# Kernel tuning notes

Hardware: AMD Instinct MI355X
Metric: run time of the kernel (lower is better)

Reference implementation:

```python
import jax, jax.numpy as jnp
import numpy as np

GROUP_SIZE = 64
SCALING = 1.0  # lora_alpha / r = 16 / 16
# bitsandbytes NF4 codebook (16 normal-float levels)
NF4_CODE = jnp.array([
    -1.0, -0.6961928009986877, -0.5250730514526367, -0.39491748809814453,
    -0.28444138169288635, -0.18477343022823334, -0.09105003625154495, 0.0,
    0.07958029955625534, 0.16093020141124725, 0.24611230194568634,
    0.33791524171829224, 0.44070982933044434, 0.5626170039176941,
    0.7229568362236023, 1.0], dtype=jnp.float32)

IN_F, OUT_F, R, TOKENS = 4096, 11008, 16, 32


def setup_inputs() -> dict:
    key = jax.random.key(0)
    k0, k1, k2, k3, k4 = jax.random.split(key, 5)
    x = jax.random.normal(k0, (TOKENS, IN_F), dtype=jnp.float32)
    # each byte packs two 4-bit NF4 indices (high nibble first)
    packed_weight = jax.random.randint(k1, (OUT_F * IN_F // 2,), 0, 256, dtype=jnp.int32)
    # per-group absmax scales (positive)
    scales = jax.random.uniform(k2, (OUT_F * IN_F // GROUP_SIZE,), dtype=jnp.float32,
                                minval=0.005, maxval=0.05)
    lora_A = jax.random.normal(k3, (R, IN_F), dtype=jnp.float32) * 0.02
    lora_B = jax.random.normal(k4, (OUT_F, R), dtype=jnp.float32) * 0.02
    return {"x": x, "packed_weight": packed_weight, "scales": scales,
            "lora_A": lora_A, "lora_B": lora_B}


def _dequant_nf4(packed_weight, scales):
    hi = packed_weight // 16          # first nibble
    lo = packed_weight % 16           # second nibble
    idx = jnp.stack([hi, lo], axis=-1).reshape(-1)          # [out*in]
    w = NF4_CODE[idx].reshape(-1, GROUP_SIZE) * scales[:, None]
    return w.reshape(OUT_F, IN_F)                            # [out, in]


def reference(x, packed_weight, scales, lora_A, lora_B):
    W = _dequant_nf4(packed_weight, scales)
    base = x @ W.T                                           # [tokens, out]
    lora = (x @ lora_A.T) @ lora_B.T                         # low-rank update
    return base + SCALING * lora
```

## Files before the change

### kernel.cpp

```cpp
#include <hip/hip_runtime.h>
#include <hip/hip_bf16.h>

#define IN_F 4096
#define OUT_F 11008
#define TOKENS 32
#define RANK 16
#define KSPLIT 8
#define KSLICE (IN_F / KSPLIT)
#define XPAD 520
#define OUT_ELEMS (TOKENS * OUT_F)

typedef unsigned short u16;
typedef __attribute__((ext_vector_type(8))) short bf16x8;
typedef __attribute__((ext_vector_type(4))) float f32x4;
typedef __attribute__((ext_vector_type(4))) int i32x4;

__device__ const float NF4_d[16] = {
    -1.0f, -0.6961928009986877f, -0.5250730514526367f, -0.39491748809814453f,
    -0.28444138169288635f, -0.18477343022823334f, -0.09105003625154495f, 0.0f,
    0.07958029955625534f, 0.16093020141124725f, 0.24611230194568634f,
    0.33791524171829224f, 0.44070982933044434f, 0.5626170039176941f,
    0.7229568362236023f, 1.0f};

static __device__ __forceinline__ unsigned pk2(float a, float b) {
    __hip_bfloat162 h = __float22bfloat162_rn(make_float2(a, b));
    unsigned u;
    __builtin_memcpy(&u, &h, 4);
    return u;
}

__global__ void prep_xa_zero(const float* __restrict__ x, const float* __restrict__ A,
                             float* __restrict__ xa, float* __restrict__ out) {
    __shared__ float red[256];
    if (blockIdx.x >= 512) {
        int i = (blockIdx.x - 512) * 256 + threadIdx.x;
        float4 z = make_float4(0.f, 0.f, 0.f, 0.f);
        for (int j = i; j < OUT_ELEMS / 4; j += 16384) ((float4*)out)[j] = z;
        return;
    }
    int b = blockIdx.x;
    int t = b >> 4, r = b & 15;
    const float4* xr = (const float4*)(x + t * IN_F);
    const float4* ar = (const float4*)(A + r * IN_F);
    float s = 0.f;
    for (int c = 0; c < 4; ++c) {
        int j = c * 256 + threadIdx.x;
        float4 xv = xr[j], av = ar[j];
        s += xv.x * av.x + xv.y * av.y + xv.z * av.z + xv.w * av.w;
    }
    red[threadIdx.x] = s;
    __syncthreads();
    for (int st = 128; st > 0; st >>= 1) {
        if (threadIdx.x < st) red[threadIdx.x] += red[threadIdx.x + st];
        __syncthreads();
    }
    if (threadIdx.x == 0) xa[b] = red[0];
}

__global__ __launch_bounds__(256, 4) void qlora_fused(
    const int* __restrict__ packed, const float* __restrict__ scales,
    const float* __restrict__ x, const float* __restrict__ xa,
    const float* __restrict__ B, float* __restrict__ out) {
    __shared__ u16 xs[32 * XPAD];
    __shared__ unsigned tbl[256];
    __shared__ float xal[512];
    const int tid = threadIdx.x;
    const int kbase = blockIdx.y * KSLICE;
    const int obase = blockIdx.x * 64;

    const int lane = tid & 63;
    const int wv = tid >> 6;
    const int n = lane & 15;
    const int q = lane >> 4;
    const int o = obase + wv * 16 + n;

    const i32x4* ppq = (const i32x4*)(packed + o * 2048 + (kbase >> 1)) + q;
    i32x4 P[4];
    P[0] = __builtin_nontemporal_load(ppq);
    P[1] = __builtin_nontemporal_load(ppq + 4);
    P[2] = __builtin_nontemporal_load(ppq + 8);
    P[3] = __builtin_nontemporal_load(ppq + 12);

    const float4* sp = (const float4*)(scales + o * 64 + (kbase >> 6));
    float4 sA = sp[0], sB = sp[1];

    tbl[tid] = pk2(NF4_d[tid & 15], NF4_d[tid >> 4]);

    if (blockIdx.y == 0) {
        xal[tid] = xa[tid];
        xal[tid + 256] = xa[tid + 256];
    }

    for (int it = 0; it < 8; ++it) {
        int row = it * 4 + (tid >> 6);
        int c8 = tid & 63;
        const float4* src = (const float4*)(x + row * IN_F + kbase + c8 * 8);
        float4 v0 = src[0], v1 = src[1];
        uint4 d;
        d.x = pk2(v0.x, v0.y);
        d.y = pk2(v0.z, v0.w);
        d.z = pk2(v1.x, v1.y);
        d.w = pk2(v1.z, v1.w);
        *(uint4*)(xs + row * XPAD + c8 * 8) = d;
    }
    __syncthreads();

    f32x4 acc0 = {0.f, 0.f, 0.f, 0.f};
    f32x4 acc1 = {0.f, 0.f, 0.f, 0.f};
    const u16* xr0 = xs + n * XPAD + q * 8;
    const u16* xr1 = xs + (n + 16) * XPAD + q * 8;
    const float scr[8] = {sA.x, sA.y, sA.z, sA.w, sB.x, sB.y, sB.z, sB.w};

#pragma unroll
    for (int s = 0; s < 16; ++s) {
        i32x4 cur = P[s & 3];
        if (s + 4 < 16) P[s & 3] = __builtin_nontemporal_load(ppq + (s + 4) * 4);
        float sc = scr[s >> 1];

        unsigned u0 = tbl[cur[0] & 255];
        unsigned u1 = tbl[cur[1] & 255];
        unsigned u2 = tbl[cur[2] & 255];
        unsigned u3 = tbl[cur[3] & 255];
        uint4 bu;
        bu.x = pk2(__int_as_float(u0 & 0xFFFF0000u) * sc, __int_as_float(u0 << 16) * sc);
        bu.y = pk2(__int_as_float(u1 & 0xFFFF0000u) * sc, __int_as_float(u1 << 16) * sc);
        bu.z = pk2(__int_as_float(u2 & 0xFFFF0000u) * sc, __int_as_float(u2 << 16) * sc);
        bu.w = pk2(__int_as_float(u3 & 0xFFFF0000u) * sc, __int_as_float(u3 << 16) * sc);
        bf16x8 bfrag;
        __builtin_memcpy(&bfrag, &bu, 16);
        bf16x8 a0 = *(const bf16x8*)(xr0 + s * 32);
        bf16x8 a1 = *(const bf16x8*)(xr1 + s * 32);
        acc0 = __builtin_amdgcn_mfma_f32_16x16x32_bf16(a0, bfrag, acc0, 0, 0, 0);
        acc1 = __builtin_amdgcn_mfma_f32_16x16x32_bf16(a1, bfrag, acc1, 0, 0, 0);
    }

    float lora[8] = {0.f, 0.f, 0.f, 0.f, 0.f, 0.f, 0.f, 0.f};
    if (blockIdx.y == 0) {
        const float4* br = (const float4*)(B + o * RANK);
        float4 b0 = br[0], b1 = br[1], b2 = br[2], b3 = br[3];
#pragma unroll
        for (int r = 0; r < 4; ++r) {
            const float* x0 = xal + (q * 4 + r) * RANK;
            const float* x1 = xal + (q * 4 + r + 16) * RANK;
            float s0 = 0.f, s1 = 0.f;
#pragma unroll
            for (int j = 0; j < 4; ++j) {
                const float4 bj = ((const float4*)&b0)[0];
            }
            s0 = b0.x * x0[0] + b0.y * x0[1] + b0.z * x0[2] + b0.w * x0[3] +
                 b1.x * x0[4] + b1.y * x0[5] + b1.z * x0[6] + b1.w * x0[7] +
                 b2.x * x0[8] + b2.y * x0[9] + b2.z * x0[10] + b2.w * x0[11] +
                 b3.x * x0[12] + b3.y * x0[13] + b3.z * x0[14] + b3.w * x0[15];
            s1 = b0.x * x1[0] + b0.y * x1[1] + b0.z * x1[2] + b0.w * x1[3] +
                 b1.x * x1[4] + b1.y * x1[5] + b1.z * x1[6] + b1.w * x1[7] +
                 b2.x * x1[8] + b2.y * x1[9] + b2.z * x1[10] + b2.w * x1[11] +
                 b3.x * x1[12] + b3.y * x1[13] + b3.z * x1[14] + b3.w * x1[15];
            lora[r] = s0;
            lora[r + 4] = s1;
        }
    }

#pragma unroll
    for (int r = 0; r < 4; ++r) {
        int t = q * 4 + r;
        atomicAdd(out + t * OUT_F + o, acc0[r] + lora[r]);
        atomicAdd(out + (t + 16) * OUT_F + o, acc1[r] + lora[r + 4]);
    }
}

extern "C" void kernel_launch(void* const* d_in, const int* in_sizes, int n_in,
                              void* d_out, int out_size, void* d_ws, size_t ws_size,
                              hipStream_t stream) {
    const float* x = (const float*)d_in[0];
    const int* packed = (const int*)d_in[1];
    const float* scales = (const float*)d_in[2];
    const float* lora_A = (const float*)d_in[3];
    const float* lora_B = (const float*)d_in[4];
    float* out = (float*)d_out;

    float* xa = (float*)d_ws;

    prep_xa_zero<<<576, 256, 0, stream>>>(x, lora_A, xa, out);
    qlora_fused<<<dim3(OUT_F / 64, KSPLIT), 256, 0, stream>>>(packed, scales, x, xa,
                                                              lora_B, out);
}
```

Baseline: 152.2 us.

## Pre-convert x to bf16, load via LDS DMA, replace atomics with split-K reduction

```diff
diff --git a/kernel.cpp b/kernel.cpp
--- a/kernel.cpp
+++ b/kernel.cpp
@@ -9,6 +9,7 @@
 #define KSLICE (IN_F / KSPLIT)
 #define XPAD 520
 #define OUT_ELEMS (TOKENS * OUT_F)
+#define NBLK (OUT_F / 64)
 
 typedef unsigned short u16;
 typedef __attribute__((ext_vector_type(8))) short bf16x8;
@@ -29,15 +30,29 @@
     return u;
 }
 
-__global__ void prep_xa_zero(const float* __restrict__ x, const float* __restrict__ A,
-                             float* __restrict__ xa, float* __restrict__ out) {
-    __shared__ float red[256];
-    if (blockIdx.x >= 512) {
-        int i = (blockIdx.x - 512) * 256 + threadIdx.x;
+__global__ void prep_kernel(const float* __restrict__ x, const float* __restrict__ A,
+                            float* __restrict__ xa, u16* __restrict__ xb,
+                            float* __restrict__ out) {
+    if (blockIdx.x >= 528) {
+        int i = (blockIdx.x - 528) * 256 + threadIdx.x;
         float4 z = make_float4(0.f, 0.f, 0.f, 0.f);
         for (int j = i; j < OUT_ELEMS / 4; j += 16384) ((float4*)out)[j] = z;
         return;
     }
+    if (blockIdx.x >= 512) {
+        int i = (blockIdx.x - 512) * 256 + threadIdx.x;
+#pragma unroll
+        for (int j = 0; j < 8; ++j) {
+            int idx = j * 4096 + i;
+            float4 v = ((const float4*)x)[idx];
+            uint2 d;
+            d.x = pk2(v.x, v.y);
+            d.y = pk2(v.z, v.w);
+            ((uint2*)xb)[idx] = d;
+        }
+        return;
+    }
+    __shared__ float red[256];
     int b = blockIdx.x;
     int t = b >> 4, r = b & 15;
     const float4* xr = (const float4*)(x + t * IN_F);
@@ -57,10 +72,11 @@
     if (threadIdx.x == 0) xa[b] = red[0];
 }
 
+template <int MODE>
 __global__ __launch_bounds__(256, 4) void qlora_fused(
     const int* __restrict__ packed, const float* __restrict__ scales,
-    const float* __restrict__ x, const float* __restrict__ xa,
-    const float* __restrict__ B, float* __restrict__ out) {
+    const u16* __restrict__ xb, const float* __restrict__ xa,
+    const float* __restrict__ B, float* __restrict__ outp) {
     __shared__ u16 xs[32 * XPAD];
     __shared__ unsigned tbl[256];
     __shared__ float xal[512];
@@ -84,24 +100,23 @@
     const float4* sp = (const float4*)(scales + o * 64 + (kbase >> 6));
     float4 sA = sp[0], sB = sp[1];
 
-    tbl[tid] = pk2(NF4_d[tid & 15], NF4_d[tid >> 4]);
-
-    if (blockIdx.y == 0) {
+    tbl[tid] = pk2(NF4_d[tid >> 4], NF4_d[tid & 15]);
+
+    if (MODE == 1 && blockIdx.y == 0) {
         xal[tid] = xa[tid];
         xal[tid + 256] = xa[tid + 256];
     }
 
-    for (int it = 0; it < 8; ++it) {
-        int row = it * 4 + (tid >> 6);
-        int c8 = tid & 63;
-        const float4* src = (const float4*)(x + row * IN_F + kbase + c8 * 8);
-        float4 v0 = src[0], v1 = src[1];
-        uint4 d;
-        d.x = pk2(v0.x, v0.y);
-        d.y = pk2(v0.z, v0.w);
-        d.z = pk2(v1.x, v1.y);
-        d.w = pk2(v1.z, v1.w);
-        *(uint4*)(xs + row * XPAD + c8 * 8) = d;
+    {
+        const u16* src = xb + kbase + lane * 8;
+#pragma unroll
+        for (int rr = 0; rr < 8; ++rr) {
+            int row = rr * 4 + wv;
+            __builtin_amdgcn_global_load_lds(
+                (const __attribute__((address_space(1))) unsigned int*)(src + row * IN_F),
+                (__attribute__((address_space(3))) unsigned int*)(xs + row * XPAD),
+                16, 0, 0);
+        }
     }
     __syncthreads();
 
@@ -112,59 +127,110 @@
     const float scr[8] = {sA.x, sA.y, sA.z, sA.w, sB.x, sB.y, sB.z, sB.w};
 
 #pragma unroll
-    for (int s = 0; s < 16; ++s) {
-        i32x4 cur = P[s & 3];
-        if (s + 4 < 16) P[s & 3] = __builtin_nontemporal_load(ppq + (s + 4) * 4);
-        float sc = scr[s >> 1];
-
-        unsigned u0 = tbl[cur[0] & 255];
-        unsigned u1 = tbl[cur[1] & 255];
-        unsigned u2 = tbl[cur[2] & 255];
-        unsigned u3 = tbl[cur[3] & 255];
-        uint4 bu;
-        bu.x = pk2(__int_as_float(u0 & 0xFFFF0000u) * sc, __int_as_float(u0 << 16) * sc);
-        bu.y = pk2(__int_as_float(u1 & 0xFFFF0000u) * sc, __int_as_float(u1 << 16) * sc);
-        bu.z = pk2(__int_as_float(u2 & 0xFFFF0000u) * sc, __int_as_float(u2 << 16) * sc);
-        bu.w = pk2(__int_as_float(u3 & 0xFFFF0000u) * sc, __int_as_float(u3 << 16) * sc);
-        bf16x8 bfrag;
-        __builtin_memcpy(&bfrag, &bu, 16);
-        bf16x8 a0 = *(const bf16x8*)(xr0 + s * 32);
-        bf16x8 a1 = *(const bf16x8*)(xr1 + s * 32);
-        acc0 = __builtin_amdgcn_mfma_f32_16x16x32_bf16(a0, bfrag, acc0, 0, 0, 0);
-        acc1 = __builtin_amdgcn_mfma_f32_16x16x32_bf16(a1, bfrag, acc1, 0, 0, 0);
-    }
-
-    float lora[8] = {0.f, 0.f, 0.f, 0.f, 0.f, 0.f, 0.f, 0.f};
-    if (blockIdx.y == 0) {
-        const float4* br = (const float4*)(B + o * RANK);
-        float4 b0 = br[0], b1 = br[1], b2 = br[2], b3 = br[3];
+    for (int g = 0; g < 8; ++g) {
+        f32x4 p0 = {0.f, 0.f, 0.f, 0.f};
+        f32x4 p1 = {0.f, 0.f, 0.f, 0.f};
+#pragma unroll
+        for (int h = 0; h < 2; ++h) {
+            const int s = g * 2 + h;
+            i32x4 cur = P[s & 3];
+            if (s + 4 < 16) P[s & 3] = __builtin_nontemporal_load(ppq + (s + 4) * 4);
+            uint4 bu;
+            bu.x = tbl[cur[0]];
+            bu.y = tbl[cur[1]];
+            bu.z = tbl[cur[2]];
+            bu.w = tbl[cur[3]];
+            bf16x8 bfrag;
+            __builtin_memcpy(&bfrag, &bu, 16);
+            bf16x8 a0 = *(const bf16x8*)(xr0 + s * 32);
+            bf16x8 a1 = *(const bf16x8*)(xr1 + s * 32);
+            p0 = __builtin_amdgcn_mfma_f32_16x16x32_bf16(a0, bfrag, p0, 0, 0, 0);
+            p1 = __builtin_amdgcn_mfma_f32_16x16x32_bf16(a1, bfrag, p1, 0, 0, 0);
+        }
+        const float sc = scr[g];
 #pragma unroll
         for (int r = 0; r < 4; ++r) {
-            const float* x0 = xal + (q * 4 + r) * RANK;
-            const float* x1 = xal + (q * 4 + r + 16) * RANK;
-            float s0 = 0.f, s1 = 0.f;
-#pragma unroll
-            for (int j = 0; j < 4; ++j) {
-                const float4 bj = ((const float4*)&b0)[0];
+            acc0[r] = fmaf(sc, p0[r], acc0[r]);
+            acc1[r] = fmaf(sc, p1[r], acc1[r]);
+        }
+    }
+
+    if (MODE == 0) {
+        float* wp = outp + (blockIdx.y * NBLK + blockIdx.x) * 2048 + tid * 8;
+        float4 v0 = make_float4(acc0[0], acc0[1], acc0[2], acc0[3]);
+        float4 v1 = make_float4(acc1[0], acc1[1], acc1[2], acc1[3]);
+        *(float4*)wp = v0;
+        *(float4*)(wp + 4) = v1;
+    } else {
+        float lora[8] = {0.f, 0.f, 0.f, 0.f, 0.f, 0.f, 0.f, 0.f};
+        if (blockIdx.y == 0) {
+            const float4* br = (const float4*)(B + o * RANK);
+            float4 b0 = br[0], b1 = br[1], b2 = br[2], b3 = br[3];
+#pragma unroll
+            for (int r = 0; r < 4; ++r) {
+                const float* x0 = xal + (q * 4 + r) * RANK;
+                const float* x1 = xal + (q * 4 + r + 16) * RANK;
+                float s0 = b0.x * x0[0] + b0.y * x0[1] + b0.z * x0[2] + b0.w * x0[3] +
+                           b1.x * x0[4] + b1.y * x0[5] + b1.z * x0[6] + b1.w * x0[7] +
+                           b2.x * x0[8] + b2.y * x0[9] + b2.z * x0[10] + b2.w * x0[11] +
+                           b3.x * x0[12] + b3.y * x0[13] + b3.z * x0[14] + b3.w * x0[15];
+                float s1 = b0.x * x1[0] + b0.y * x1[1] + b0.z * x1[2] + b0.w * x1[3] +
+                           b1.x * x1[4] + b1.y * x1[5] + b1.z * x1[6] + b1.w * x1[7] +
+                           b2.x * x1[8] + b2.y * x1[9] + b2.z * x1[10] + b2.w * x1[11] +
+                           b3.x * x1[12] + b3.y * x1[13] + b3.z * x1[14] + b3.w * x1[15];
+                lora[r] = s0;
+                lora[r + 4] = s1;
             }
-            s0 = b0.x * x0[0] + b0.y * x0[1] + b0.z * x0[2] + b0.w * x0[3] +
-                 b1.x * x0[4] + b1.y * x0[5] + b1.z * x0[6] + b1.w * x0[7] +
-                 b2.x * x0[8] + b2.y * x0[9] + b2.z * x0[10] + b2.w * x0[11] +
-                 b3.x * x0[12] + b3.y * x0[13] + b3.z * x0[14] + b3.w * x0[15];
-            s1 = b0.x * x1[0] + b0.y * x1[1] + b0.z * x1[2] + b0.w * x1[3] +
-                 b1.x * x1[4] + b1.y * x1[5] + b1.z * x1[6] + b1.w * x1[7] +
-                 b2.x * x1[8] + b2.y * x1[9] + b2.z * x1[10] + b2.w * x1[11] +
-                 b3.x * x1[12] + b3.y * x1[13] + b3.z * x1[14] + b3.w * x1[15];
-            lora[r] = s0;
-            lora[r + 4] = s1;
-        }
-    }
-
+        }
+#pragma unroll
+        for (int r = 0; r < 4; ++r) {
+            int t = q * 4 + r;
+            atomicAdd(outp + t * OUT_F + o, acc0[r] + lora[r]);
+            atomicAdd(outp + (t + 16) * OUT_F + o, acc1[r] + lora[r + 4]);
+        }
+    }
+}
+
+__global__ __launch_bounds__(256) void reduce_out(
+    const float* __restrict__ part, const float* __restrict__ xa,
+    const float* __restrict__ B, float* __restrict__ out) {
+    __shared__ float xal[512];
+    const int tid = threadIdx.x;
+    const int bx = blockIdx.x;
+    xal[tid] = xa[tid];
+    xal[tid + 256] = xa[tid + 256];
+    __syncthreads();
+
+    const float4* p = (const float4*)part + bx * 512 + tid * 2;
+    float4 s0 = p[0], s1 = p[1];
+#pragma unroll
+    for (int s = 1; s < 8; ++s) {
+        float4 a = p[s * (NBLK * 512)];
+        float4 b = p[s * (NBLK * 512) + 1];
+        s0.x += a.x; s0.y += a.y; s0.z += a.z; s0.w += a.w;
+        s1.x += b.x; s1.y += b.y; s1.z += b.z; s1.w += b.w;
+    }
+
+    const int lane = tid & 63, wv = tid >> 6, n = lane & 15, q = lane >> 4;
+    const int o = bx * 64 + wv * 16 + n;
+    const float4* br = (const float4*)(B + o * RANK);
+    float4 b0 = br[0], b1 = br[1], b2 = br[2], b3 = br[3];
+    float res[8] = {s0.x, s0.y, s0.z, s0.w, s1.x, s1.y, s1.z, s1.w};
 #pragma unroll
     for (int r = 0; r < 4; ++r) {
-        int t = q * 4 + r;
-        atomicAdd(out + t * OUT_F + o, acc0[r] + lora[r]);
-        atomicAdd(out + (t + 16) * OUT_F + o, acc1[r] + lora[r + 4]);
+        int t0 = q * 4 + r;
+        const float* x0 = xal + t0 * RANK;
+        const float* x1 = xal + (t0 + 16) * RANK;
+        float l0 = b0.x * x0[0] + b0.y * x0[1] + b0.z * x0[2] + b0.w * x0[3] +
+                   b1.x * x0[4] + b1.y * x0[5] + b1.z * x0[6] + b1.w * x0[7] +
+                   b2.x * x0[8] + b2.y * x0[9] + b2.z * x0[10] + b2.w * x0[11] +
+                   b3.x * x0[12] + b3.y * x0[13] + b3.z * x0[14] + b3.w * x0[15];
+        float l1 = b0.x * x1[0] + b0.y * x1[1] + b0.z * x1[2] + b0.w * x1[3] +
+                   b1.x * x1[4] + b1.y * x1[5] + b1.z * x1[6] + b1.w * x1[7] +
+                   b2.x * x1[8] + b2.y * x1[9] + b2.z * x1[10] + b2.w * x1[11] +
+                   b3.x * x1[12] + b3.y * x1[13] + b3.z * x1[14] + b3.w * x1[15];
+        out[t0 * OUT_F + o] = res[r] + l0;
+        out[(t0 + 16) * OUT_F + o] = res[r + 4] + l1;
     }
 }
 
@@ -179,8 +245,19 @@
     float* out = (float*)d_out;
 
     float* xa = (float*)d_ws;
-
-    prep_xa_zero<<<576, 256, 0, stream>>>(x, lora_A, xa, out);
-    qlora_fused<<<dim3(OUT_F / 64, KSPLIT), 256, 0, stream>>>(packed, scales, x, xa,
-                                                              lora_B, out);
-}
+    u16* xb = (u16*)((char*)d_ws + 2048);
+    float* part = (float*)((char*)d_ws + 2048 + TOKENS * IN_F * 2);
+    size_t need = 2048 + (size_t)TOKENS * IN_F * 2 +
+                  (size_t)KSPLIT * NBLK * 2048 * sizeof(float);
+
+    if (ws_size >= need) {
+        prep_kernel<<<528, 256, 0, stream>>>(x, lora_A, xa, xb, out);
+        qlora_fused<0><<<dim3(NBLK, KSPLIT), 256, 0, stream>>>(packed, scales, xb, xa,
+                                                               lora_B, part);
+        reduce_out<<<NBLK, 256, 0, stream>>>(part, xa, lora_B, out);
+    } else {
+        prep_kernel<<<592, 256, 0, stream>>>(x, lora_A, xa, xb, out);
+        qlora_fused<1><<<dim3(NBLK, KSPLIT), 256, 0, stream>>>(packed, scales, xb, xa,
+                                                               lora_B, out);
+    }
+}
```

Result: no change. 154.3 us (+1.4%).
